# Performance work log

Hardware: AMD Instinct MI355X
Metric: run time of the kernel (lower is better)

The kernel has to match this reference:

```python
import jax, jax.numpy as jnp
import numpy as np

B = 4096; NINP = 512; NHID = 2048; NB = 8; BS = 256  # block_size_out
ATT_OUT = 4 * BS; TOPK = 4; DK_I = 64; NH = 4; DK_M = 16


def setup_inputs() -> dict:
    ks = jax.random.split(jax.random.key(0), 16)
    g = lambda i, shape, s=0.01: s * jax.random.normal(ks[i], shape, dtype=jnp.float32)
    return dict(
        inp=jax.random.normal(ks[0], (B, NINP), dtype=jnp.float32),
        hx=jax.random.normal(ks[1], (B, NHID), dtype=jnp.float32),
        cx=jax.random.normal(ks[2], (B, NHID), dtype=jnp.float32),
        # inp_att group-linear projections (GroupLinearLayer init 0.01*randn)
        Wq_i=g(3, (NB, BS, DK_I)), Wk_i=g(4, (2, NINP, DK_I)), Wv_i=g(5, (2, NINP, ATT_OUT)),
        # mha group-linear projections (4 heads * d_k=16)
        Wq_m=g(6, (NB, BS, NH * DK_M)), Wk_m=g(7, (NB, BS, NH * DK_M)), Wv_m=g(8, (NB, BS, NH * DK_M)),
        fc_w=g(9, (BS, NH * DK_M), 0.05), fc_b=jnp.zeros((BS,), jnp.float32),
        gate_w=g(10, (BS, NH * DK_M), 0.05), gate_b=jnp.zeros((BS,), jnp.float32),
        # blockified LSTMCell: k=NB independent (ATT_OUT -> BS) cells, gate order i,f,g,o
        Wih=g(11, (NB, 4 * BS, ATT_OUT), 0.02), Whh=g(12, (NB, 4 * BS, BS), 0.05),
        b_ih=jnp.zeros((NB, 4 * BS), jnp.float32), b_hh=jnp.zeros((NB, 4 * BS), jnp.float32),
        step=0,
    )


def _fwd(inp, hx, cx, Wq_i, Wk_i, Wv_i, Wq_m, Wk_m, Wv_m, fc_w, fc_b, gate_w, gate_b, Wih, Whh, b_ih, b_hh):
    b = inp.shape[0]
    # input read: concat null slot + input (num_blocks_in=1, num_modules_read_input=2)
    x = inp.reshape(b, 1, NINP)
    x = jnp.concatenate([jnp.zeros_like(x), x], axis=1)  # (b, 2, NINP); slot 0 = null
    hq = hx.reshape(b, NB, BS)
    q = jnp.einsum('bkd,kde->bke', hq, Wq_i)              # (b, NB, DK_I)
    k = jnp.einsum('bkd,kde->bke', x, Wk_i)               # (b, 2, DK_I)
    v = jnp.einsum('bkd,kde->bke', x, Wv_i)               # (b, 2, ATT_OUT)
    iatt = jax.nn.softmax(jnp.einsum('bqe,bke->bqk', q, k) / jnp.sqrt(jnp.float32(DK_I)), axis=-1)
    inp_use = jnp.einsum('bqk,bke->bqe', iatt, v)         # (b, NB, ATT_OUT); skip_write => identity fc
    # top-k selection: blocks with HIGHEST null-attention get frozen (masked out)
    _, botk = jax.lax.top_k(iatt[:, :, 0], NB - TOPK)
    mblk = jnp.ones((b, NB), inp.dtype).at[jnp.arange(b)[:, None], botk].set(0.0)
    mblk = jax.lax.stop_gradient(mblk)                    # mask.detach()
    mask = jnp.repeat(mblk, BS, axis=1)                   # (b, NHID)
    # block-diagonal LSTM cell (post blockify_params)
    hb = hx.reshape(b, NB, BS); cb = cx.reshape(b, NB, BS)
    gates = jnp.einsum('bkd,kgd->bkg', inp_use, Wih) + jnp.einsum('bkh,kgh->bkg', hb, Whh) + b_ih + b_hh
    ig, fg, gg, og = jnp.split(gates, 4, axis=-1)
    c_new = jax.nn.sigmoid(fg) * cb + jax.nn.sigmoid(ig) * jnp.tanh(gg)
    h_new = jax.nn.sigmoid(og) * jnp.tanh(c_new)          # (b, NB, BS)
    # step attention among blocks; blocked_grad: forward identity, backward masked
    m3 = mblk[:, :, None]
    hg = m3 * h_new + jax.lax.stop_gradient((1.0 - m3) * h_new)
    qm = jnp.einsum('bkd,kde->bke', hg, Wq_m).reshape(b, NB, NH, DK_M)
    km = jnp.einsum('bkd,kde->bke', hg, Wk_m).reshape(b, NB, NH, DK_M)
    vm = jnp.einsum('bkd,kde->bke', hg, Wv_m).reshape(b, NB, NH, DK_M)
    a = jax.nn.softmax(jnp.einsum('bqhe,bkhe->bhqk', qm, km) / jnp.sqrt(jnp.float32(DK_M)), axis=-1)
    o = jnp.einsum('bhqk,bkhe->bqhe', a, vm).reshape(b, NB, NH * DK_M)
    att_out = jax.nn.sigmoid(o @ gate_w.T + gate_b) * jnp.tanh(o @ fc_w.T + fc_b)  # residual gating
    h_new = (h_new + att_out).reshape(b, NHID)
    c_new = c_new.reshape(b, NHID)
    hx_out = mask * h_new + (1.0 - mask) * hx
    cx_out = mask * c_new + (1.0 - mask) * cx
    return hx_out, cx_out, mask


def reference(inp, hx, cx, Wq_i, Wk_i, Wv_i, Wq_m, Wk_m, Wv_m, fc_w, fc_b, gate_w, gate_b, Wih, Whh, b_ih, b_hh, step):
    return _fwd(inp, hx, cx, Wq_i, Wk_i, Wv_i, Wq_m, Wk_m, Wv_m, fc_w, fc_b, gate_w, gate_b, Wih, Whh, b_ih, b_hh)
```

## Files before the change

kernel.cpp:

```cpp
#include <hip/hip_runtime.h>
#include <hip/hip_bf16.h>


#define B_SZ 4096
#define NINP 512
#define NHID 2048
#define NB 8
#define BSZ 256
#define ATT_OUT 1024

typedef __attribute__((ext_vector_type(8))) short bf16x8;
typedef __attribute__((ext_vector_type(8))) unsigned short u16x8;
typedef __attribute__((ext_vector_type(4))) float f32x4;

__device__ __forceinline__ float sigf(float x) { return 1.0f / (1.0f + expf(-x)); }

__device__ __forceinline__ unsigned short f2bf(float x) {
    unsigned u = __float_as_uint(x);
    unsigned r = (u + 0x7fff + ((u >> 16) & 1)) >> 16;
    return (unsigned short)r;
}
__device__ __forceinline__ float bf2f(unsigned short u) {
    return __uint_as_float((unsigned)u << 16);
}

__device__ __forceinline__ void gload16(const void* g, void* l) {
    __builtin_amdgcn_global_load_lds(
        (const __attribute__((address_space(1))) unsigned int*)(unsigned long long)g,
        (__attribute__((address_space(3))) unsigned int*)(unsigned int)(unsigned long long)l,
        16, 0, 0);
}

__device__ __forceinline__ u16x8 cvt8(const float4& a, const float4& b) {
    u16x8 v;
    v[0] = f2bf(a.x); v[1] = f2bf(a.y); v[2] = f2bf(a.z); v[3] = f2bf(a.w);
    v[4] = f2bf(b.x); v[5] = f2bf(b.y); v[6] = f2bf(b.z); v[7] = f2bf(b.w);
    return v;
}

__global__ __launch_bounds__(256) void prep1_kernel(
    const float* __restrict__ gw, const float* __restrict__ fw,
    unsigned short* __restrict__ Wgfb,
    const float4* __restrict__ hx4, u16x8* __restrict__ hxb8,
    const float4* __restrict__ inp4, u16x8* __restrict__ inpb8,
    const float4* __restrict__ Wv4, u16x8* __restrict__ Wvb8)
{
    const int bid = blockIdx.x;
    if (bid < 128) {
        int t = bid * 256 + threadIdx.x;
        Wgfb[t] = f2bf((t < 16384) ? gw[t] : fw[t - 16384]);
    } else if (bid < 4224) {
        long i = (long)(bid - 128) * 256 + threadIdx.x;
        hxb8[i] = cvt8(hx4[i * 2], hx4[i * 2 + 1]);
    } else if (bid < 5248) {
        long i = (long)(bid - 4224) * 256 + threadIdx.x;
        inpb8[i] = cvt8(inp4[i * 2], inp4[i * 2 + 1]);
    } else {
        long i = (long)(bid - 5248) * 256 + threadIdx.x;
        Wvb8[i] = cvt8(Wv4[i * 2], Wv4[i * 2 + 1]);
    }
}

__global__ __launch_bounds__(256) void prepW_kernel(
    const float4* __restrict__ Wih4, u16x8* __restrict__ Wihb8,
    const float4* __restrict__ Whh4, u16x8* __restrict__ Whhb8)
{
    const int bid = blockIdx.x;
    if (bid < 4096) {
        long i = (long)bid * 256 + threadIdx.x;
        Wihb8[i] = cvt8(Wih4[i * 2], Wih4[i * 2 + 1]);
    } else {
        long i = (long)(bid - 4096) * 256 + threadIdx.x;
        Whhb8[i] = cvt8(Whh4[i * 2], Whh4[i * 2 + 1]);
    }
}

__global__ __launch_bounds__(256) void qkvw_kernel(
    const float* __restrict__ Wq, const float* __restrict__ Wk,
    const float* __restrict__ Wv, unsigned short* __restrict__ out)
{
    int idx = blockIdx.x * 256 + threadIdx.x;
    int k = idx & 255;
    int n = (idx >> 8) % 192;
    int kb = idx / (192 * 256);
    const float* src = (n < 64) ? Wq : (n < 128) ? Wk : Wv;
    int nn = n & 63;
    out[idx] = f2bf(src[(long)kb * 16384 + k * 64 + nn]);
}

__global__ __launch_bounds__(256) void qk1_kernel(
    const float* __restrict__ inp, const float* __restrict__ hx,
    const float* __restrict__ Wk1, const float* __restrict__ Wq,
    float* __restrict__ k1, float* __restrict__ q)
{
    const int role = blockIdx.y;
    const int m0 = blockIdx.x * 32;
    const float* A; long lda; const float* Bw; int K; float* C; int ldc;
    if (role == 8) {
        A = inp + (long)m0 * 512; lda = 512; Bw = Wk1; K = 512;
        C = k1 + (long)m0 * 64; ldc = 64;
    } else {
        A = hx + (long)m0 * 2048 + role * 256; lda = 2048;
        Bw = Wq + (long)role * 256 * 64; K = 256;
        C = q + (long)m0 * 512 + role * 64; ldc = 512;
    }

    __shared__ float As[32][33];
    __shared__ float Bs[32][64];

    const int t = threadIdx.x;
    const int ty = t >> 4;
    const int tx = t & 15;

    float acc[2][4] = {};

    for (int k0 = 0; k0 < K; k0 += 32) {
        {
            int m = t >> 3, kk = (t & 7) << 2;
            float4 av = *reinterpret_cast<const float4*>(&A[(long)m * lda + k0 + kk]);
            As[m][kk] = av.x; As[m][kk + 1] = av.y;
            As[m][kk + 2] = av.z; As[m][kk + 3] = av.w;
        }
        #pragma unroll
        for (int u = 0; u < 2; ++u) {
            int f = t + 256 * u;
            int kr = f >> 4, c = (f & 15) << 2;
            float4 bv = *reinterpret_cast<const float4*>(&Bw[(long)(k0 + kr) * 64 + c]);
            *reinterpret_cast<float4*>(&Bs[kr][c]) = bv;
        }
        __syncthreads();
        #pragma unroll
        for (int kk = 0; kk < 32; ++kk) {
            float a0 = As[ty * 2][kk];
            float a1 = As[ty * 2 + 1][kk];
            float4 bv = *reinterpret_cast<const float4*>(&Bs[kk][tx * 4]);
            acc[0][0] += a0 * bv.x; acc[0][1] += a0 * bv.y;
            acc[0][2] += a0 * bv.z; acc[0][3] += a0 * bv.w;
            acc[1][0] += a1 * bv.x; acc[1][1] += a1 * bv.y;
            acc[1][2] += a1 * bv.z; acc[1][3] += a1 * bv.w;
        }
        __syncthreads();
    }
    #pragma unroll
    for (int i = 0; i < 2; ++i) {
        float4 v = {acc[i][0], acc[i][1], acc[i][2], acc[i][3]};
        *reinterpret_cast<float4*>(&C[(long)(ty * 2 + i) * ldc + tx * 4]) = v;
    }
}

__global__ __launch_bounds__(256, 2) void gemm_mfma_bf(
    const unsigned short* __restrict__ A,
    const unsigned short* __restrict__ Bm,
    unsigned short* __restrict__ Cv,
    int K, int lda, int ldb, int ldc,
    long aOffZ, long bOffZ, long cOffZ)
{
    const int m0 = blockIdx.x * 128;
    const int n0 = blockIdx.y * 64;
    const int z = blockIdx.z;
    A += (long)z * aOffZ;
    Bm += (long)z * bOffZ;

    __shared__ unsigned short As[128 * 64];
    __shared__ unsigned short Bs[64 * 64];

    const int t = threadIdx.x;
    const int wid = t >> 6;
    const int l = t & 63;
    const int l15 = l & 15;
    const int l4 = l >> 4;
    const int wm = wid >> 1;
    const int wn = wid & 1;

    f32x4 acc[4][2];
    #pragma unroll
    for (int m = 0; m < 4; ++m)
        #pragma unroll
        for (int n = 0; n < 2; ++n)
            acc[m][n] = (f32x4){0.f, 0.f, 0.f, 0.f};

    for (int k0 = 0; k0 < K; k0 += 64) {
        #pragma unroll
        for (int s = 0; s < 4; ++s) {
            int ci = (wid * 4 + s) * 64 + l;
            int r = ci >> 3, cs = ci & 7;
            gload16(A + (long)(m0 + r) * lda + k0 + ((cs ^ (r & 7)) << 3), &As[ci * 8]);
        }
        #pragma unroll
        for (int s = 0; s < 2; ++s) {
            int ci = (wid * 2 + s) * 64 + l;
            int rn = ci >> 3, cs = ci & 7;
            gload16(Bm + (long)(n0 + rn) * ldb + k0 + ((cs ^ (rn & 7)) << 3), &Bs[ci * 8]);
        }
        __syncthreads();
        #pragma unroll
        for (int kh = 0; kh < 2; ++kh) {
            bf16x8 af[4];
            #pragma unroll
            for (int m = 0; m < 4; ++m) {
                int r = wm * 64 + m * 16 + l15;
                int c = kh * 4 + l4;
                af[m] = *reinterpret_cast<const bf16x8*>(&As[r * 64 + ((c ^ (r & 7)) << 3)]);
            }
            #pragma unroll
            for (int nf = 0; nf < 2; ++nf) {
                int rn = wn * 32 + nf * 16 + l15;
                int c = kh * 4 + l4;
                bf16x8 bf = *reinterpret_cast<const bf16x8*>(
                    &Bs[rn * 64 + ((c ^ (rn & 7)) << 3)]);
                #pragma unroll
                for (int m = 0; m < 4; ++m)
                    acc[m][nf] = __builtin_amdgcn_mfma_f32_16x16x32_bf16(
                        af[m], bf, acc[m][nf], 0, 0, 0);
            }
        }
        __syncthreads();
    }

    #pragma unroll
    for (int nf = 0; nf < 2; ++nf) {
        const int ccol = n0 + wn * 32 + nf * 16 + l15;
        #pragma unroll
        for (int m = 0; m < 4; ++m) {
            #pragma unroll
            for (int r = 0; r < 4; ++r) {
                const long crow = m0 + wm * 64 + m * 16 + l4 * 4 + r;
                Cv[(long)z * cOffZ + crow * ldc + ccol] = f2bf(acc[m][nf][r]);
            }
        }
    }
}

__global__ __launch_bounds__(256) void s1_mask_kernel(
    const float* __restrict__ q, const float* __restrict__ k1,
    float* __restrict__ w_ws, float* __restrict__ mblk,
    float* __restrict__ mask_out)
{
    const int wave = threadIdx.x >> 6;
    const int lane = threadIdx.x & 63;
    const int b = blockIdx.x * 4 + wave;

    float p[8];
    const float kv = k1[(long)b * 64 + lane];
    #pragma unroll
    for (int kb = 0; kb < 8; ++kb)
        p[kb] = q[(long)b * 512 + kb * 64 + lane] * kv;

    #pragma unroll
    for (int off = 1; off < 64; off <<= 1) {
        #pragma unroll
        for (int kb = 0; kb < 8; ++kb) p[kb] += __shfl_xor(p[kb], off);
    }

    float s[8], mv[8];
    #pragma unroll
    for (int kb = 0; kb < 8; ++kb) s[kb] = p[kb] * 0.125f;

    #pragma unroll
    for (int j = 0; j < 8; ++j) {
        int r = 0;
        #pragma unroll
        for (int i = 0; i < 8; ++i)
            r += (s[i] < s[j]) || (s[i] == s[j] && i < j);
        mv[j] = (r >= 4) ? 1.0f : 0.0f;
    }
    if (lane < 8) {
        w_ws[(long)b * 8 + lane] = sigf(s[lane]);
        mblk[(long)b * 8 + lane] = mv[lane];
    }
    #pragma unroll
    for (int it = 0; it < 8; ++it) {
        const float mvv = mv[it];
        float4 v = {mvv, mvv, mvv, mvv};
        *reinterpret_cast<float4*>(&mask_out[(long)b * 2048 + it * 256 + lane * 4]) = v;
    }
}

__global__ __launch_bounds__(256, 2) void gates_mfma_kernel(
    const unsigned short* __restrict__ Ib,
    const unsigned short* __restrict__ Hb,
    const unsigned short* __restrict__ Gt,
    const unsigned short* __restrict__ Whhb,
    const float* __restrict__ b_ih, const float* __restrict__ b_hh,
    const float* __restrict__ w_ws, const float* __restrict__ mblk,
    const float* __restrict__ cx,
    float* __restrict__ c_out,
    unsigned short* __restrict__ hn_b)
{
    const int n = blockIdx.x + 32 * blockIdx.y + 128 * blockIdx.z;
    const int w = (n & 7) * 128 + (n >> 3);
    const int m0 = ((w >> 2) & 31) * 128;
    const int j0 = (w & 3) * 64;
    const int kb = w >> 7;

    __shared__ unsigned short As[128 * 64];
    __shared__ unsigned short Bs[256 * 64];
    __shared__ float wv[128];
    __shared__ float mbs[128];

    const int t = threadIdx.x;
    const int wid = t >> 6;
    const int l = t & 63;
    const int l15 = l & 15;
    const int l4 = l >> 4;
    const int wm = wid >> 1;
    const int wj = wid & 1;

    if (t < 128) {
        wv[t] = w_ws[(long)(m0 + t) * 8 + kb];
        mbs[t] = mblk[(long)(m0 + t) * 8 + kb];
    }

    f32x4 acc[4][8];
    #pragma unroll
    for (int m = 0; m < 4; ++m)
        #pragma unroll
        for (int nn = 0; nn < 8; ++nn)
            acc[m][nn] = (f32x4){0.f, 0.f, 0.f, 0.f};

    auto stage = [&](const unsigned short* Aptr, long lda,
                     const unsigned short* Bptr, long ldb, int k0) {
        #pragma unroll
        for (int s = 0; s < 4; ++s) {
            int ci = (wid * 4 + s) * 64 + l;
            int r = ci >> 3, cs = ci & 7;
            const unsigned short* g = Aptr + (long)r * lda + k0 + ((cs ^ (r & 7)) << 3);
            gload16(g, &As[ci * 8]);
        }
        #pragma unroll
        for (int s = 0; s < 8; ++s) {
            int ci = (wid * 8 + s) * 64 + l;
            int rn = ci >> 3, cs = ci & 7;
            int sg = rn >> 6, jl = rn & 63;
            const unsigned short* g = Bptr + (long)(sg * 256 + j0 + jl) * ldb + k0
                                      + ((cs ^ (rn & 7)) << 3);
            gload16(g, &Bs[ci * 8]);
        }
    };

    auto compute = [&]() {
        #pragma unroll
        for (int kh = 0; kh < 2; ++kh) {
            bf16x8 af[4];
            #pragma unroll
            for (int m = 0; m < 4; ++m) {
                int r = wm * 64 + m * 16 + l15;
                int c = kh * 4 + l4;
                af[m] = *reinterpret_cast<const bf16x8*>(&As[r * 64 + ((c ^ (r & 7)) << 3)]);
            }
            #pragma unroll
            for (int sg = 0; sg < 4; ++sg) {
                #pragma unroll
                for (int jf = 0; jf < 2; ++jf) {
                    int rn = sg * 64 + wj * 32 + jf * 16 + l15;
                    int c = kh * 4 + l4;
                    bf16x8 bf = *reinterpret_cast<const bf16x8*>(
                        &Bs[rn * 64 + ((c ^ (rn & 7)) << 3)]);
                    #pragma unroll
                    for (int m = 0; m < 4; ++m)
                        acc[m][sg * 2 + jf] = __builtin_amdgcn_mfma_f32_16x16x32_bf16(
                            af[m], bf, acc[m][sg * 2 + jf], 0, 0, 0);
                }
            }
        }
    };

    {
        const unsigned short* A1 = Ib + (long)m0 * 512;
        const unsigned short* B1 = Gt + (long)kb * 1024 * 512;
        for (int k0 = 0; k0 < 512; k0 += 64) {
            stage(A1, 512, B1, 512, k0);
            __syncthreads();
            compute();
            __syncthreads();
        }
    }

    {
        float wsc[4][4];
        #pragma unroll
        for (int m = 0; m < 4; ++m)
            #pragma unroll
            for (int r = 0; r < 4; ++r)
                wsc[m][r] = wv[wm * 64 + m * 16 + l4 * 4 + r];
        #pragma unroll
        for (int m = 0; m < 4; ++m)
            #pragma unroll
            for (int nn = 0; nn < 8; ++nn)
                #pragma unroll
                for (int r = 0; r < 4; ++r)
                    acc[m][nn][r] *= wsc[m][r];
    }

    {
        const unsigned short* A2 = Hb + (long)m0 * 2048 + kb * 256;
        const unsigned short* B2 = Whhb + (long)kb * 1024 * 256;
        for (int k0 = 0; k0 < 256; k0 += 64) {
            stage(A2, 2048, B2, 256, k0);
            __syncthreads();
            compute();
            __syncthreads();
        }
    }

    #pragma unroll
    for (int jf = 0; jf < 2; ++jf) {
        const int jcol = j0 + wj * 32 + jf * 16 + l15;
        const long bb = (long)kb * 1024 + jcol;
        const float bI = b_ih[bb] + b_hh[bb];
        const float bF = b_ih[bb + 256] + b_hh[bb + 256];
        const float bG = b_ih[bb + 512] + b_hh[bb + 512];
        const float bO = b_ih[bb + 768] + b_hh[bb + 768];
        #pragma unroll
        for (int m = 0; m < 4; ++m) {
            #pragma unroll
            for (int r = 0; r < 4; ++r) {
                const long row = m0 + wm * 64 + m * 16 + l4 * 4 + r;
                const long idx = row * 2048 + kb * 256 + jcol;
                const float mv = mbs[wm * 64 + m * 16 + l4 * 4 + r];
                const float ig = acc[m][0 + jf][r] + bI;
                const float fg = acc[m][2 + jf][r] + bF;
                const float gg = acc[m][4 + jf][r] + bG;
                const float og = acc[m][6 + jf][r] + bO;
                const float co = cx[idx];
                const float cn = sigf(fg) * co + sigf(ig) * tanhf(gg);
                const float hn = sigf(og) * tanhf(cn);
                c_out[idx] = (mv != 0.0f) ? cn : co;
                hn_b[idx] = f2bf(hn);
            }
        }
    }
}

__global__ __launch_bounds__(256) void attn_m2_kernel(
    const unsigned short* __restrict__ qkv, unsigned short* __restrict__ ob)
{
    const int tid = blockIdx.x * 256 + threadIdx.x;
    const int b = tid >> 5;
    const int qkb = (tid >> 2) & 7;
    const int h = tid & 3;
    const u16x8* base8 = reinterpret_cast<const u16x8*>(qkv + (long)b * 1536);

    float qv[16];
    {
        u16x8 q0 = base8[qkb * 24 + h * 2];
        u16x8 q1 = base8[qkb * 24 + h * 2 + 1];
        #pragma unroll
        for (int e = 0; e < 8; ++e) { qv[e] = bf2f(q0[e]); qv[8 + e] = bf2f(q1[e]); }
    }

    float sc[8];
    float mx = -1e30f;
    #pragma unroll
    for (int kk = 0; kk < 8; ++kk) {
        u16x8 k0 = base8[kk * 24 + 8 + h * 2];
        u16x8 k1 = base8[kk * 24 + 9 + h * 2];
        float s = 0.f;
        #pragma unroll
        for (int e = 0; e < 8; ++e)
            s += qv[e] * bf2f(k0[e]) + qv[8 + e] * bf2f(k1[e]);
        s *= 0.25f;
        sc[kk] = s;
        mx = fmaxf(mx, s);
    }
    float den = 0.f;
    #pragma unroll
    for (int kk = 0; kk < 8; ++kk) { sc[kk] = expf(sc[kk] - mx); den += sc[kk]; }
    const float inv = 1.0f / den;

    float ov[16] = {};
    #pragma unroll
    for (int kk = 0; kk < 8; ++kk) {
        const float pw = sc[kk] * inv;
        u16x8 v0 = base8[kk * 24 + 16 + h * 2];
        u16x8 v1 = base8[kk * 24 + 17 + h * 2];
        #pragma unroll
        for (int e = 0; e < 8; ++e) {
            ov[e] += pw * bf2f(v0[e]);
            ov[8 + e] += pw * bf2f(v1[e]);
        }
    }
    u16x8 r0, r1;
    #pragma unroll
    for (int e = 0; e < 8; ++e) { r0[e] = f2bf(ov[e]); r1[e] = f2bf(ov[e + 8]); }
    unsigned short* op = ob + (long)((b * 8 + qkb) * 64 + h * 16);
    *reinterpret_cast<u16x8*>(op) = r0;
    *reinterpret_cast<u16x8*>(op + 8) = r1;
}

__global__ __launch_bounds__(256) void attn_final_kernel(
    const unsigned short* __restrict__ ob,
    const unsigned short* __restrict__ Wgfb,
    const float* __restrict__ gate_b, const float* __restrict__ fc_b,
    const float* __restrict__ mblk,
    const float* __restrict__ hx,
    const unsigned short* __restrict__ hnb,
    float* __restrict__ h_out)
{
    const int m0 = blockIdx.x * 128;
    const int j0 = blockIdx.y * 64;

    __shared__ unsigned short As[128 * 64];
    __shared__ unsigned short Bs[128 * 64];

    const int t = threadIdx.x;
    const int wid = t >> 6;
    const int l = t & 63;
    const int l15 = l & 15;
    const int l4 = l >> 4;
    const int wm = wid >> 1;
    const int wn = wid & 1;

    #pragma unroll
    for (int s = 0; s < 4; ++s) {
        int ci = (wid * 4 + s) * 64 + l;
        int r = ci >> 3, cs = ci & 7;
        gload16(ob + (long)(m0 + r) * 64 + ((cs ^ (r & 7)) << 3), &As[ci * 8]);
    }
    #pragma unroll
    for (int s = 0; s < 4; ++s) {
        int ci = (wid * 4 + s) * 64 + l;
        int r = ci >> 3, cs = ci & 7;
        int n = (r < 64) ? (j0 + r) : (256 + j0 + (r - 64));
        gload16(Wgfb + (long)n * 64 + ((cs ^ (r & 7)) << 3), &Bs[ci * 8]);
    }
    __syncthreads();

    f32x4 acc[4][2][2];
    #pragma unroll
    for (int m = 0; m < 4; ++m)
        #pragma unroll
        for (int nf = 0; nf < 2; ++nf)
            #pragma unroll
            for (int gf = 0; gf < 2; ++gf)
                acc[m][nf][gf] = (f32x4){0.f, 0.f, 0.f, 0.f};

    #pragma unroll
    for (int kh = 0; kh < 2; ++kh) {
        const int c = kh * 4 + l4;
        bf16x8 af[4];
        #pragma unroll
        for (int m = 0; m < 4; ++m) {
            int r = wm * 64 + m * 16 + l15;
            af[m] = *reinterpret_cast<const bf16x8*>(&As[r * 64 + ((c ^ (r & 7)) << 3)]);
        }
        #pragma unroll
        for (int nf = 0; nf < 2; ++nf) {
            int rg = wn * 32 + nf * 16 + l15;
            bf16x8 bg = *reinterpret_cast<const bf16x8*>(
                &Bs[rg * 64 + ((c ^ (rg & 7)) << 3)]);
            int rf = 64 + rg;
            bf16x8 bfv = *reinterpret_cast<const bf16x8*>(
                &Bs[rf * 64 + ((c ^ (rf & 7)) << 3)]);
            #pragma unroll
            for (int m = 0; m < 4; ++m) {
                acc[m][nf][0] = __builtin_amdgcn_mfma_f32_16x16x32_bf16(
                    af[m], bg, acc[m][nf][0], 0, 0, 0);
                acc[m][nf][1] = __builtin_amdgcn_mfma_f32_16x16x32_bf16(
                    af[m], bfv, acc[m][nf][1], 0, 0, 0);
            }
        }
    }

    #pragma unroll
    for (int nf = 0; nf < 2; ++nf) {
        const int j = j0 + wn * 32 + nf * 16 + l15;
        const float gb = gate_b[j];
        const float fb = fc_b[j];
        #pragma unroll
        for (int m = 0; m < 4; ++m) {
            #pragma unroll
            for (int r = 0; r < 4; ++r) {
                const long p = m0 + wm * 64 + m * 16 + l4 * 4 + r;
                const float g = acc[m][nf][0][r] + gb;
                const float f = acc[m][nf][1][r] + fb;
                const float att = sigf(g) * tanhf(f);
                const long idx = (p >> 3) * 2048 + (p & 7) * 256 + j;
                const float mv = mblk[p];
                const float hn = bf2f(hnb[idx]) + att;
                h_out[idx] = (mv != 0.0f) ? hn : hx[idx];
            }
        }
    }
}

extern "C" void kernel_launch(void* const* d_in, const int* in_sizes, int n_in,
                              void* d_out, int out_size, void* d_ws, size_t ws_size,
                              hipStream_t stream) {
    const float* inp    = (const float*)d_in[0];
    const float* hx     = (const float*)d_in[1];
    const float* cx     = (const float*)d_in[2];
    const float* Wq_i   = (const float*)d_in[3];
    const float* Wk_i   = (const float*)d_in[4];
    const float* Wv_i   = (const float*)d_in[5];
    const float* Wq_m   = (const float*)d_in[6];
    const float* Wk_m   = (const float*)d_in[7];
    const float* Wv_m   = (const float*)d_in[8];
    const float* fc_w   = (const float*)d_in[9];
    const float* fc_b   = (const float*)d_in[10];
    const float* gate_w = (const float*)d_in[11];
    const float* gate_b = (const float*)d_in[12];
    const float* Wih    = (const float*)d_in[13];
    const float* Whh    = (const float*)d_in[14];
    const float* b_ih   = (const float*)d_in[15];
    const float* b_hh   = (const float*)d_in[16];

    float* out      = (float*)d_out;
    float* h_out    = out;
    float* c_out    = out + (long)B_SZ * 2048;
    float* mask_out = out + (long)2 * B_SZ * 2048;

    float* ws   = (float*)d_ws;
    float* w_ws = ws;
    float* mblk = w_ws + (long)B_SZ * 8;
    unsigned short* Gt  = (unsigned short*)(mblk + (long)B_SZ * 8);
    unsigned short* hxb = Gt + (long)8 * 1024 * 512;
    unsigned short* hnb  = hxb + (long)B_SZ * 2048;
    unsigned short* Wihb = hnb + (long)B_SZ * 2048;
    unsigned short* Whhb = Wihb + (long)8 * 1024 * 1024;
    unsigned short* Wgfb = Whhb + (long)8 * 1024 * 256;
    float* k1 = (float*)Wihb;
    float* q  = k1 + (long)B_SZ * 64;
    unsigned short* Wvb = hnb;
    unsigned short* inpb = (unsigned short*)h_out;
    unsigned short* Wqkvb = Wihb;
    unsigned short* qkvb  = hxb;
    unsigned short* ob    = (unsigned short*)Gt;

    prep1_kernel<<<dim3(5504), 256, 0, stream>>>(
        gate_w, fc_w, Wgfb,
        (const float4*)hx, (u16x8*)hxb,
        (const float4*)inp, (u16x8*)inpb,
        (const float4*)(Wv_i + (long)NINP * ATT_OUT), (u16x8*)Wvb);
    qk1_kernel<<<dim3(128, 9), 256, 0, stream>>>(
        inp, hx, Wk_i + (long)NINP * 64, Wq_i, k1, q);
    s1_mask_kernel<<<dim3(B_SZ / 4), 256, 0, stream>>>(q, k1, w_ws, mblk, mask_out);
    prepW_kernel<<<dim3(5120), 256, 0, stream>>>(
        (const float4*)Wih, (u16x8*)Wihb, (const float4*)Whh, (u16x8*)Whhb);
    gemm_mfma_bf<<<dim3(8, 8, 8), 256, 0, stream>>>(
        Wihb, Wvb, Gt, 1024, 1024, 1024, 512,
        (long)1024 * 1024, 0, (long)1024 * 512);
    gates_mfma_kernel<<<dim3(B_SZ / 128, 4, 8), 256, 0, stream>>>(
        inpb, hxb, Gt, Whhb, b_ih, b_hh, w_ws, mblk, cx, c_out, hnb);
    qkvw_kernel<<<dim3(1536), 256, 0, stream>>>(Wq_m, Wk_m, Wv_m, Wqkvb);
    gemm_mfma_bf<<<dim3(32, 3, 8), 256, 0, stream>>>(
        hnb, Wqkvb, qkvb, 256, 2048, 256, 1536, 256, (long)192 * 256, 192);
    attn_m2_kernel<<<dim3(B_SZ * 32 / 256), 256, 0, stream>>>(qkvb, ob);
    attn_final_kernel<<<dim3(256, 4), 256, 0, stream>>>(
        ob, Wgfb, gate_b, fc_b, mblk, hx, hnb, h_out);
}
```

Measured before the change: 235.0 us.

## Double-buffer LDS in gates kernel and enlarge tile to 256 rows with 512 threads

The gates GEMM kernel now uses 512-thread blocks covering 256 batch rows each, which halves the grid and lets each block reuse its loaded weight tile across twice as many rows. Its two K-loops (input-projection and recurrent) become one 12-step loop with double-buffered shared memory, so the next tile is prefetched while the current one is computed and one barrier per step is removed. The cost is double the LDS footprint (about 128KB per block), which limits blocks per CU and may stop the requested two blocks per CU from fitting. Fewer blocks also means less parallelism to fill the GPU.

```diff
diff --git a/kernel.cpp b/kernel.cpp
--- a/kernel.cpp
+++ b/kernel.cpp
@@ -276,7 +276,7 @@
     }
 }
 
-__global__ __launch_bounds__(256, 2) void gates_mfma_kernel(
+__global__ __launch_bounds__(512, 2) void gates_mfma_kernel(
     const unsigned short* __restrict__ Ib,
     const unsigned short* __restrict__ Hb,
     const unsigned short* __restrict__ Gt,
@@ -287,16 +287,16 @@
     float* __restrict__ c_out,
     unsigned short* __restrict__ hn_b)
 {
-    const int n = blockIdx.x + 32 * blockIdx.y + 128 * blockIdx.z;
-    const int w = (n & 7) * 128 + (n >> 3);
-    const int m0 = ((w >> 2) & 31) * 128;
+    const int n = blockIdx.x + 16 * blockIdx.y + 64 * blockIdx.z;
+    const int w = (n & 7) * 64 + (n >> 3);
+    const int m0 = ((w >> 2) & 15) * 256;
     const int j0 = (w & 3) * 64;
-    const int kb = w >> 7;
-
-    __shared__ unsigned short As[128 * 64];
-    __shared__ unsigned short Bs[256 * 64];
-    __shared__ float wv[128];
-    __shared__ float mbs[128];
+    const int kb = w >> 6;
+
+    __shared__ unsigned short Asm[2][256 * 64];
+    __shared__ unsigned short Bsm[2][256 * 64];
+    __shared__ float wv[256];
+    __shared__ float mbs[256];
 
     const int t = threadIdx.x;
     const int wid = t >> 6;
@@ -306,7 +306,7 @@
     const int wm = wid >> 1;
     const int wj = wid & 1;
 
-    if (t < 128) {
+    if (t < 256) {
         wv[t] = w_ws[(long)(m0 + t) * 8 + kb];
         mbs[t] = mblk[(long)(m0 + t) * 8 + kb];
     }
@@ -318,27 +318,39 @@
         for (int nn = 0; nn < 8; ++nn)
             acc[m][nn] = (f32x4){0.f, 0.f, 0.f, 0.f};
 
-    auto stage = [&](const unsigned short* Aptr, long lda,
-                     const unsigned short* Bptr, long ldb, int k0) {
+    auto stage = [&](int step, int buf) {
+        const unsigned short* Aptr; long lda;
+        const unsigned short* Bptr; long ldb; int k0;
+        if (step < 8) {
+            Aptr = Ib + (long)m0 * 512; lda = 512;
+            Bptr = Gt + (long)kb * 1024 * 512; ldb = 512;
+            k0 = step * 64;
+        } else {
+            Aptr = Hb + (long)m0 * 2048 + kb * 256; lda = 2048;
+            Bptr = Whhb + (long)kb * 1024 * 256; ldb = 256;
+            k0 = (step - 8) * 64;
+        }
+        unsigned short* Al = Asm[buf];
+        unsigned short* Bl = Bsm[buf];
         #pragma unroll
         for (int s = 0; s < 4; ++s) {
-            int ci = (wid * 4 + s) * 64 + l;
+            int ci = wid * 256 + s * 64 + l;
             int r = ci >> 3, cs = ci & 7;
-            const unsigned short* g = Aptr + (long)r * lda + k0 + ((cs ^ (r & 7)) << 3);
-            gload16(g, &As[ci * 8]);
-        }
-        #pragma unroll
-        for (int s = 0; s < 8; ++s) {
-            int ci = (wid * 8 + s) * 64 + l;
+            gload16(Aptr + (long)r * lda + k0 + ((cs ^ (r & 7)) << 3), &Al[ci * 8]);
+        }
+        #pragma unroll
+        for (int s = 0; s < 4; ++s) {
+            int ci = wid * 256 + s * 64 + l;
             int rn = ci >> 3, cs = ci & 7;
             int sg = rn >> 6, jl = rn & 63;
-            const unsigned short* g = Bptr + (long)(sg * 256 + j0 + jl) * ldb + k0
-                                      + ((cs ^ (rn & 7)) << 3);
-            gload16(g, &Bs[ci * 8]);
+            gload16(Bptr + (long)(sg * 256 + j0 + jl) * ldb + k0 + ((cs ^ (rn & 7)) << 3),
+                    &Bl[ci * 8]);
         }
     };
 
-    auto compute = [&]() {
+    auto compute = [&](int buf) {
+        const unsigned short* Al = Asm[buf];
+        const unsigned short* Bl = Bsm[buf];
         #pragma unroll
         for (int kh = 0; kh < 2; ++kh) {
             bf16x8 af[4];
@@ -346,7 +358,7 @@
             for (int m = 0; m < 4; ++m) {
                 int r = wm * 64 + m * 16 + l15;
                 int c = kh * 4 + l4;
-                af[m] = *reinterpret_cast<const bf16x8*>(&As[r * 64 + ((c ^ (r & 7)) << 3)]);
+                af[m] = *reinterpret_cast<const bf16x8*>(&Al[r * 64 + ((c ^ (r & 7)) << 3)]);
             }
             #pragma unroll
             for (int sg = 0; sg < 4; ++sg) {
@@ -355,7 +367,7 @@
                     int rn = sg * 64 + wj * 32 + jf * 16 + l15;
                     int c = kh * 4 + l4;
                     bf16x8 bf = *reinterpret_cast<const bf16x8*>(
-                        &Bs[rn * 64 + ((c ^ (rn & 7)) << 3)]);
+                        &Bl[rn * 64 + ((c ^ (rn & 7)) << 3)]);
                     #pragma unroll
                     for (int m = 0; m < 4; ++m)
                         acc[m][sg * 2 + jf] = __builtin_amdgcn_mfma_f32_16x16x32_bf16(
@@ -365,42 +377,29 @@
         }
     };
 
-    {
-        const unsigned short* A1 = Ib + (long)m0 * 512;
-        const unsigned short* B1 = Gt + (long)kb * 1024 * 512;
-        for (int k0 = 0; k0 < 512; k0 += 64) {
-            stage(A1, 512, B1, 512, k0);
-            __syncthreads();
-            compute();
-            __syncthreads();
-        }
-    }
-
-    {
-        float wsc[4][4];
-        #pragma unroll
-        for (int m = 0; m < 4; ++m)
-            #pragma unroll
-            for (int r = 0; r < 4; ++r)
-                wsc[m][r] = wv[wm * 64 + m * 16 + l4 * 4 + r];
-        #pragma unroll
-        for (int m = 0; m < 4; ++m)
-            #pragma unroll
-            for (int nn = 0; nn < 8; ++nn)
+    stage(0, 0);
+    __syncthreads();
+    int cur = 0;
+    for (int step = 0; step < 12; ++step) {
+        if (step < 11) stage(step + 1, cur ^ 1);
+        compute(cur);
+        if (step == 7) {
+            float wsc[4][4];
+            #pragma unroll
+            for (int m = 0; m < 4; ++m)
                 #pragma unroll
                 for (int r = 0; r < 4; ++r)
-                    acc[m][nn][r] *= wsc[m][r];
-    }
-
-    {
-        const unsigned short* A2 = Hb + (long)m0 * 2048 + kb * 256;
-        const unsigned short* B2 = Whhb + (long)kb * 1024 * 256;
-        for (int k0 = 0; k0 < 256; k0 += 64) {
-            stage(A2, 2048, B2, 256, k0);
-            __syncthreads();
-            compute();
-            __syncthreads();
-        }
+                    wsc[m][r] = wv[wm * 64 + m * 16 + l4 * 4 + r];
+            #pragma unroll
+            for (int m = 0; m < 4; ++m)
+                #pragma unroll
+                for (int nn = 0; nn < 8; ++nn)
+                    #pragma unroll
+                    for (int r = 0; r < 4; ++r)
+                        acc[m][nn][r] *= wsc[m][r];
+        }
+        __syncthreads();
+        cur ^= 1;
     }
 
     #pragma unroll
@@ -640,7 +639,7 @@
     gemm_mfma_bf<<<dim3(8, 8, 8), 256, 0, stream>>>(
         Wihb, Wvb, Gt, 1024, 1024, 1024, 512,
         (long)1024 * 1024, 0, (long)1024 * 512);
-    gates_mfma_kernel<<<dim3(B_SZ / 128, 4, 8), 256, 0, stream>>>(
+    gates_mfma_kernel<<<dim3(16, 4, 8), 512, 0, stream>>>(
         inpb, hxb, Gt, Whhb, b_ih, b_hh, w_ws, mblk, cx, c_out, hnb);
     qkvw_kernel<<<dim3(1536), 256, 0, stream>>>(Wq_m, Wk_m, Wv_m, Wqkvb);
     gemm_mfma_bf<<<dim3(32, 3, 8), 256, 0, stream>>>(
```

Measured after the change: 240.4 us. 1.02x slower.
